# Kernel tuning notes

Measured on AMD Instinct MI355X. Metric: run time of the kernel, lower is better.

The kernel has to match this reference:

```python
import jax, jax.numpy as jnp
import numpy as np

N_NODES = 20000
N_EDGES = 320000
IN_F = 168
HID = 256


def gcn_conv(x, W, b, src, dst, ew, n_nodes):
    """PyG GCNConv: symmetric normalization with self-loops (fill 1.0).
    out = D^-1/2 (A + I) D^-1/2 X W^T + b, aggregated at dst (source_to_target).
    """
    xw = x @ W.T  # [N, F_out]
    # degree at target nodes, including self-loop weight 1.0
    deg = jax.ops.segment_sum(ew, dst, num_segments=n_nodes) + 1.0
    dinv = jnp.where(deg > 0, jax.lax.rsqrt(deg), 0.0)
    norm = dinv[src] * ew * dinv[dst]  # [E]
    agg = jax.ops.segment_sum(norm[:, None] * xw[src], dst, num_segments=n_nodes)
    # self-loop contribution: norm_ii = dinv[i]^2
    out = agg + (dinv * dinv)[:, None] * xw
    return out + b


def setup_inputs() -> dict:
    key = jax.random.key(0)
    k = jax.random.split(key, 8)
    x = jax.random.normal(k[0], (N_NODES, IN_F), dtype=jnp.float32)
    edge_index = jax.random.randint(k[1], (2, N_EDGES), 0, N_NODES, dtype=jnp.int64)
    edge_weight = jax.random.uniform(k[2], (N_EDGES,), dtype=jnp.float32)
    # GCN layer weights (PyG Linear: y = x W^T), plus per-layer bias
    s1 = 1.0 / np.sqrt(IN_F)
    s2 = 1.0 / np.sqrt(HID)
    W1 = jax.random.uniform(k[3], (HID, IN_F), minval=-s1, maxval=s1, dtype=jnp.float32)
    b1 = jnp.zeros((HID,), dtype=jnp.float32)
    W2 = jax.random.uniform(k[4], (HID, HID), minval=-s2, maxval=s2, dtype=jnp.float32)
    b2 = jnp.zeros((HID,), dtype=jnp.float32)
    return {"x": x, "edge_index": edge_index, "edge_weight": edge_weight,
            "W1": W1, "b1": b1, "W2": W2, "b2": b2}


def reference(x, edge_index, edge_weight, W1, b1, W2, b2):
    src, dst = edge_index[0], edge_index[1]
    h = gcn_conv(x, W1, b1, src, dst, edge_weight, N_NODES)
    h = jax.nn.relu(h)
    h = gcn_conv(h, W2, b2, src, dst, edge_weight, N_NODES)
    h = jax.nn.relu(h)
    return h
```

## Files before the change

### kernel.cpp

```cpp
#include <hip/hip_runtime.h>

#define N_NODES 20000
#define N_EDGES 320000
#define IN_F    168
#define HID     256
#define K1P     192
#define XS      192
#define NF4     42
#define X4      48
#define CAP     96
#define E2      (N_EDGES / 2)

typedef __attribute__((ext_vector_type(8))) short bf16x8;
typedef __attribute__((ext_vector_type(4))) float f32x4;
typedef __attribute__((ext_vector_type(2))) float f32x2;

__device__ __forceinline__ short f2bf(float f) {
    union { float f; unsigned u; } v; v.f = f;
    unsigned r = v.u + 0x7FFFu + ((v.u >> 16) & 1u);
    return (short)(r >> 16);
}
__device__ __forceinline__ f32x2 bfp(unsigned u) {
    f32x2 r;
    r.x = __uint_as_float(u << 16);
    r.y = __uint_as_float(u & 0xFFFF0000u);
    return r;
}

__global__ void prep_all(const float* __restrict__ x, short* __restrict__ xb,
                         const float* __restrict__ W1, const float* __restrict__ W2,
                         short* __restrict__ w1b, short* __restrict__ w2b,
                         const int* __restrict__ ei, const float* __restrict__ ew,
                         float* __restrict__ deg, int* __restrict__ counts) {
    const int xTot  = N_NODES * X4;
    const int w1Tot = 256 * X4;
    const int w2Tot = 256 * 64;
    int i = blockIdx.x * 256 + threadIdx.x;
    if (i < xTot) {
        int n  = i / X4;
        int k4 = i - n * X4;
        short4 o;
        if (k4 < NF4) {
            float4 v = *(const float4*)(x + (size_t)n * IN_F + k4 * 4);
            o = make_short4(f2bf(v.x), f2bf(v.y), f2bf(v.z), f2bf(v.w));
        } else {
            o = make_short4(0, 0, 0, 0);
        }
        *(short4*)(xb + (size_t)n * XS + k4 * 4) = o;
        return;
    }
    i -= xTot;
    if (i < w1Tot) {
        int r  = i / X4;
        int k4 = i - r * X4;
        short4 o;
        if (k4 < NF4) {
            float4 v = *(const float4*)(W1 + (size_t)r * IN_F + k4 * 4);
            o = make_short4(f2bf(v.x), f2bf(v.y), f2bf(v.z), f2bf(v.w));
        } else {
            o = make_short4(0, 0, 0, 0);
        }
        *(short4*)(w1b + (size_t)r * K1P + k4 * 4) = o;
        return;
    }
    i -= w1Tot;
    if (i < w2Tot) {
        int r  = i >> 6;
        int c4 = i & 63;
        float4 v = *(const float4*)(W2 + (size_t)r * HID + c4 * 4);
        *(short4*)(w2b + (size_t)r * HID + c4 * 4) =
            make_short4(f2bf(v.x), f2bf(v.y), f2bf(v.z), f2bf(v.w));
        return;
    }
    i -= w2Tot;
    if (i < N_EDGES) {
        int d = ei[N_EDGES + i];
        atomicAdd(&deg[d], ew[i]);
        atomicAdd(&counts[d], 1);
    }
}

__global__ void scatter_edges(const int* __restrict__ ei, const float* __restrict__ ew,
                              const float* __restrict__ deg,
                              const int* __restrict__ counts,
                              int* __restrict__ cursor, int2* __restrict__ er) {
    int t = blockIdx.x * 256 + threadIdx.x;
    if (t < E2) {
        int2   s2 = *(const int2*)(ei + 2 * t);
        int2   d2 = *(const int2*)(ei + N_EDGES + 2 * t);
        float2 w2 = *(const float2*)(ew + 2 * t);
        float nm0 = rsqrtf(deg[s2.x] + 1.0f) * w2.x * rsqrtf(deg[d2.x] + 1.0f);
        int c0 = atomicAdd(&cursor[d2.x], 1);
        if (c0 < CAP) er[d2.x * CAP + c0] = make_int2(s2.x, __float_as_int(nm0));
        float nm1 = rsqrtf(deg[s2.y] + 1.0f) * w2.y * rsqrtf(deg[d2.y] + 1.0f);
        int c1 = atomicAdd(&cursor[d2.y], 1);
        if (c1 < CAP) er[d2.y * CAP + c1] = make_int2(s2.y, __float_as_int(nm1));
        return;
    }
    int n = t - E2;
    if (n < N_NODES) {
        int base = n * CAP;
        int p   = base + counts[n];
        int end = base + ((counts[n] + 7) & ~7);
        for (; p < end; ++p) er[p] = make_int2(0, 0);
    }
}


__global__ __launch_bounds__(256) void agg_x(const short* __restrict__ xb,
                                             const float* __restrict__ deg,
                                             const int* __restrict__ counts,
                                             const int2* __restrict__ er,
                                             short* __restrict__ ax) {
    int wave = threadIdx.x >> 6;
    int lane = threadIdx.x & 63;
    int n = blockIdx.x * 4 + wave;
    bool act = lane < NF4;
    int lo4 = act ? lane * 4 : 0;
    float di = rsqrtf(deg[n] + 1.0f);
    float sw = di * di;
    uint2 sv = *(const uint2*)(xb + (size_t)n * XS + lo4);
    f32x2 a01 = bfp(sv.x) * sw;
    f32x2 a23 = bfp(sv.y) * sw;

    int p0 = n * CAP;
    int p1 = p0 + ((counts[n] + 7) & ~7);
    for (int p = p0; p < p1; p += 8) {
        const int4* e4 = (const int4*)(er + p);
        int4 eA = e4[0], eB = e4[1], eC = e4[2], eD = e4[3];
        uint2 r0 = *(const uint2*)(xb + (size_t)eA.x * XS + lo4);
        uint2 r1 = *(const uint2*)(xb + (size_t)eA.z * XS + lo4);
        uint2 r2 = *(const uint2*)(xb + (size_t)eB.x * XS + lo4);
        uint2 r3 = *(const uint2*)(xb + (size_t)eB.z * XS + lo4);
        uint2 r4 = *(const uint2*)(xb + (size_t)eC.x * XS + lo4);
        uint2 r5 = *(const uint2*)(xb + (size_t)eC.z * XS + lo4);
        uint2 r6 = *(const uint2*)(xb + (size_t)eD.x * XS + lo4);
        uint2 r7 = *(const uint2*)(xb + (size_t)eD.z * XS + lo4);
        float w0 = __int_as_float(eA.y), w1 = __int_as_float(eA.w);
        float w2 = __int_as_float(eB.y), w3 = __int_as_float(eB.w);
        float w4 = __int_as_float(eC.y), w5 = __int_as_float(eC.w);
        float w6 = __int_as_float(eD.y), w7 = __int_as_float(eD.w);
        a01 += bfp(r0.x) * w0; a23 += bfp(r0.y) * w0;
        a01 += bfp(r1.x) * w1; a23 += bfp(r1.y) * w1;
        a01 += bfp(r2.x) * w2; a23 += bfp(r2.y) * w2;
        a01 += bfp(r3.x) * w3; a23 += bfp(r3.y) * w3;
        a01 += bfp(r4.x) * w4; a23 += bfp(r4.y) * w4;
        a01 += bfp(r5.x) * w5; a23 += bfp(r5.y) * w5;
        a01 += bfp(r6.x) * w6; a23 += bfp(r6.y) * w6;
        a01 += bfp(r7.x) * w7; a23 += bfp(r7.y) * w7;
    }

    size_t base = (size_t)n * K1P + lane * 4;
    if (act) {
        *(short4*)&ax[base] = make_short4(f2bf(a01.x), f2bf(a01.y),
                                          f2bf(a23.x), f2bf(a23.y));
    } else if (lane < 48) {
        *(short4*)&ax[base] = make_short4(0, 0, 0, 0);
    }
}

__global__ __launch_bounds__(256) void agg_h(const short* __restrict__ h1h,
                                             const float* __restrict__ deg,
                                             const int* __restrict__ counts,
                                             const int2* __restrict__ er,
                                             short* __restrict__ ah) {
    int wave = threadIdx.x >> 6;
    int lane = threadIdx.x & 63;
    int n = blockIdx.x * 4 + wave;
    int lo4 = lane * 4;
    float di = rsqrtf(deg[n] + 1.0f);
    float sw = di * di;
    uint2 sv = *(const uint2*)(h1h + (size_t)n * HID + lo4);
    f32x2 a01 = bfp(sv.x) * sw;
    f32x2 a23 = bfp(sv.y) * sw;

    int p0 = n * CAP;
    int p1 = p0 + ((counts[n] + 7) & ~7);
    for (int p = p0; p < p1; p += 8) {
        const int4* e4 = (const int4*)(er + p);
        int4 eA = e4[0], eB = e4[1], eC = e4[2], eD = e4[3];
        uint2 r0 = *(const uint2*)(h1h + (size_t)eA.x * HID + lo4);
        uint2 r1 = *(const uint2*)(h1h + (size_t)eA.z * HID + lo4);
        uint2 r2 = *(const uint2*)(h1h + (size_t)eB.x * HID + lo4);
        uint2 r3 = *(const uint2*)(h1h + (size_t)eB.z * HID + lo4);
        uint2 r4 = *(const uint2*)(h1h + (size_t)eC.x * HID + lo4);
        uint2 r5 = *(const uint2*)(h1h + (size_t)eC.z * HID + lo4);
        uint2 r6 = *(const uint2*)(h1h + (size_t)eD.x * HID + lo4);
        uint2 r7 = *(const uint2*)(h1h + (size_t)eD.z * HID + lo4);
        float w0 = __int_as_float(eA.y), w1 = __int_as_float(eA.w);
        float w2 = __int_as_float(eB.y), w3 = __int_as_float(eB.w);
        float w4 = __int_as_float(eC.y), w5 = __int_as_float(eC.w);
        float w6 = __int_as_float(eD.y), w7 = __int_as_float(eD.w);
        a01 += bfp(r0.x) * w0; a23 += bfp(r0.y) * w0;
        a01 += bfp(r1.x) * w1; a23 += bfp(r1.y) * w1;
        a01 += bfp(r2.x) * w2; a23 += bfp(r2.y) * w2;
        a01 += bfp(r3.x) * w3; a23 += bfp(r3.y) * w3;
        a01 += bfp(r4.x) * w4; a23 += bfp(r4.y) * w4;
        a01 += bfp(r5.x) * w5; a23 += bfp(r5.y) * w5;
        a01 += bfp(r6.x) * w6; a23 += bfp(r6.y) * w6;
        a01 += bfp(r7.x) * w7; a23 += bfp(r7.y) * w7;
    }

    *(short4*)&ah[(size_t)n * HID + lo4] = make_short4(f2bf(a01.x), f2bf(a01.y),
                                                       f2bf(a23.x), f2bf(a23.y));
}

#define LDS_STRIDE 72

__global__ __launch_bounds__(256) void gemm_bf(const short* __restrict__ Ah,
                                               const short* __restrict__ Wh,
                                               const float* __restrict__ bias,
                                               float* __restrict__ Cf,
                                               short* __restrict__ Cbf,
                                               int M, int Ks, int nsteps, int mode) {
    __shared__ short sAh[64 * LDS_STRIDE];
    __shared__ short sWh[64 * LDS_STRIDE];

    const int idx   = blockIdx.x;
    const int group = idx >> 5;
    const int xcd   = idx & 7;
    const int slot  = (idx >> 3) & 3;
    const int mt    = group * 8 + xcd;
    const int mtiles = (M + 63) >> 6;
    if (mt >= mtiles) return;
    const int bm = mt * 64;
    const int bn = slot * 64;

    const int tid  = threadIdx.x;
    const int lane = tid & 63;
    const int wv   = tid >> 6;
    const int l16  = lane & 15;
    const int quad = lane >> 4;
    const int wm   = (wv & 1) * 32;
    const int wn   = (wv >> 1) * 32;

    const int srow = tid >> 2;
    const int sseg = (tid & 3) * 16;
    int arow = bm + srow; if (arow >= M) arow = M - 1;
    const short* gAh = Ah + (size_t)arow * Ks;
    const short* gWh = Wh + (size_t)(bn + srow) * Ks;
    const int lds_off = srow * LDS_STRIDE + sseg;

    f32x4 acc00 = {0,0,0,0}, acc01 = {0,0,0,0}, acc10 = {0,0,0,0}, acc11 = {0,0,0,0};

    int4 pah0 = *(const int4*)(gAh + sseg), pah1 = *(const int4*)(gAh + sseg + 8);
    int4 pwh0 = *(const int4*)(gWh + sseg), pwh1 = *(const int4*)(gWh + sseg + 8);

    for (int ks = 0; ks < nsteps; ++ks) {
        *(int4*)&sAh[lds_off] = pah0; *(int4*)&sAh[lds_off + 8] = pah1;
        *(int4*)&sWh[lds_off] = pwh0; *(int4*)&sWh[lds_off + 8] = pwh1;
        __syncthreads();
        if (ks + 1 < nsteps) {
            int o = (ks + 1) * 64 + sseg;
            pah0 = *(const int4*)(gAh + o); pah1 = *(const int4*)(gAh + o + 8);
            pwh0 = *(const int4*)(gWh + o); pwh1 = *(const int4*)(gWh + o + 8);
        }
        #pragma unroll
        for (int o = 0; o < 2; ++o) {
            const int a0 = (wm + l16) * LDS_STRIDE + o * 32 + quad * 8;
            const int a1 = a0 + 16 * LDS_STRIDE;
            const int w0 = (wn + l16) * LDS_STRIDE + o * 32 + quad * 8;
            const int w1 = w0 + 16 * LDS_STRIDE;
            bf16x8 ah0 = *(const bf16x8*)&sAh[a0];
            bf16x8 ah1 = *(const bf16x8*)&sAh[a1];
            bf16x8 wh0 = *(const bf16x8*)&sWh[w0];
            bf16x8 wh1 = *(const bf16x8*)&sWh[w1];
            acc00 = __builtin_amdgcn_mfma_f32_16x16x32_bf16(ah0, wh0, acc00, 0, 0, 0);
            acc01 = __builtin_amdgcn_mfma_f32_16x16x32_bf16(ah0, wh1, acc01, 0, 0, 0);
            acc10 = __builtin_amdgcn_mfma_f32_16x16x32_bf16(ah1, wh0, acc10, 0, 0, 0);
            acc11 = __builtin_amdgcn_mfma_f32_16x16x32_bf16(ah1, wh1, acc11, 0, 0, 0);
        }
        __syncthreads();
    }

    const int colb = bn + wn + l16;
    const int rowb = bm + wm + quad * 4;
    const float b0 = bias[colb];
    const float b1 = bias[colb + 16];
    #pragma unroll
    for (int r = 0; r < 4; ++r) {
        int row = rowb + r;
        if (row < M) {
            float v0 = acc00[r] + b0; v0 = v0 > 0.f ? v0 : 0.f;
            float v1 = acc01[r] + b1; v1 = v1 > 0.f ? v1 : 0.f;
            if (mode == 0) {
                Cbf[(size_t)row * HID + colb]      = f2bf(v0);
                Cbf[(size_t)row * HID + colb + 16] = f2bf(v1);
            } else {
                Cf[(size_t)row * HID + colb]      = v0;
                Cf[(size_t)row * HID + colb + 16] = v1;
            }
        }
        int row2 = row + 16;
        if (row2 < M) {
            float v0 = acc10[r] + b0; v0 = v0 > 0.f ? v0 : 0.f;
            float v1 = acc11[r] + b1; v1 = v1 > 0.f ? v1 : 0.f;
            if (mode == 0) {
                Cbf[(size_t)row2 * HID + colb]      = f2bf(v0);
                Cbf[(size_t)row2 * HID + colb + 16] = f2bf(v1);
            } else {
                Cf[(size_t)row2 * HID + colb]      = v0;
                Cf[(size_t)row2 * HID + colb + 16] = v1;
            }
        }
    }
}


extern "C" void kernel_launch(void* const* d_in, const int* in_sizes, int n_in,
                              void* d_out, int out_size, void* d_ws, size_t ws_size,
                              hipStream_t stream) {
    const float* x  = (const float*)d_in[0];
    const int*   ei = (const int*)d_in[1];
    const float* ew = (const float*)d_in[2];
    const float* W1 = (const float*)d_in[3];
    const float* b1 = (const float*)d_in[4];
    const float* W2 = (const float*)d_in[5];
    const float* b2 = (const float*)d_in[6];
    float* out = (float*)d_out;

    char* ws = (char*)d_ws;
    float* deg      = (float*)(ws);
    int*   counts   = (int*)(ws + 80000);
    int*   cursor   = (int*)(ws + 160000);
    int2*  er       = (int2*)(ws + 240000);
    short* ax       = (short*)(ws + 15600000);
    short* ah       = (short*)(ws + 15600000);
    short* h1h      = (short*)(ws + 25840000);
    short* w1b      = (short*)(ws + 36080000);
    short* w2b      = (short*)(ws + 36178304);
    short* xb       = (short*)(ws + 36309376);

    hipMemsetAsync(d_ws, 0, 240000, stream);

    const int prep_tot = N_NODES * X4 + 256 * X4 + 256 * 64 + N_EDGES;
    prep_all<<<(prep_tot + 255) / 256, 256, 0, stream>>>(
        x, xb, W1, W2, w1b, w2b, ei, ew, deg, counts);
    const int sc_blocks = (E2 + N_NODES + 255) / 256;
    scatter_edges<<<sc_blocks, 256, 0, stream>>>(ei, ew, deg, counts, cursor, er);

    const int mtiles = (N_NODES + 63) / 64;
    const int gemm_grid = ((mtiles + 7) / 8) * 32;

    agg_x<<<N_NODES / 4, 256, 0, stream>>>(xb, deg, counts, er, ax);
    gemm_bf<<<gemm_grid, 256, 0, stream>>>(ax, w1b, b1, nullptr, h1h,
                                           N_NODES, K1P, 3, 0);
    agg_h<<<N_NODES / 4, 256, 0, stream>>>(h1h, deg, counts, er, ah);
    gemm_bf<<<gemm_grid, 256, 0, stream>>>(ah, w2b, b2, out, nullptr,
                                           N_NODES, HID, 4, 1);
}
```

Baseline: 191.7 us.

## Fuse neighbor aggregation with dense GEMM per 16-row tile for both layers

Replaces the separate aggregate kernels and tiled GEMM kernels with two fused kernels. Each block aggregates 16 nodes into LDS as bf16 and then multiplies them by the weight matrix with MFMA, reading weight fragments directly from global memory. This removes the round trip of the aggregated matrices through global memory and cuts two kernel launches. In exchange, weights are re-read by every block without LDS staging, and each wave now processes its 4 rows sequentially, which reduces gather parallelism.

New measurement: 207.5 us. 1.08x slower.

```diff
diff --git a/kernel.cpp b/kernel.cpp
--- a/kernel.cpp
+++ b/kernel.cpp
@@ -10,6 +10,8 @@
 #define X4      48
 #define CAP     96
 #define E2      (N_EDGES / 2)
+#define ASTR1   200
+#define ASTR2   264
 
 typedef __attribute__((ext_vector_type(8))) short bf16x8;
 typedef __attribute__((ext_vector_type(4))) float f32x4;
@@ -106,203 +108,186 @@
     }
 }
 
-
-__global__ __launch_bounds__(256) void agg_x(const short* __restrict__ xb,
-                                             const float* __restrict__ deg,
-                                             const int* __restrict__ counts,
-                                             const int2* __restrict__ er,
-                                             short* __restrict__ ax) {
-    int wave = threadIdx.x >> 6;
-    int lane = threadIdx.x & 63;
-    int n = blockIdx.x * 4 + wave;
-    bool act = lane < NF4;
-    int lo4 = act ? lane * 4 : 0;
-    float di = rsqrtf(deg[n] + 1.0f);
-    float sw = di * di;
-    uint2 sv = *(const uint2*)(xb + (size_t)n * XS + lo4);
-    f32x2 a01 = bfp(sv.x) * sw;
-    f32x2 a23 = bfp(sv.y) * sw;
-
-    int p0 = n * CAP;
-    int p1 = p0 + ((counts[n] + 7) & ~7);
-    for (int p = p0; p < p1; p += 8) {
-        const int4* e4 = (const int4*)(er + p);
-        int4 eA = e4[0], eB = e4[1], eC = e4[2], eD = e4[3];
-        uint2 r0 = *(const uint2*)(xb + (size_t)eA.x * XS + lo4);
-        uint2 r1 = *(const uint2*)(xb + (size_t)eA.z * XS + lo4);
-        uint2 r2 = *(const uint2*)(xb + (size_t)eB.x * XS + lo4);
-        uint2 r3 = *(const uint2*)(xb + (size_t)eB.z * XS + lo4);
-        uint2 r4 = *(const uint2*)(xb + (size_t)eC.x * XS + lo4);
-        uint2 r5 = *(const uint2*)(xb + (size_t)eC.z * XS + lo4);
-        uint2 r6 = *(const uint2*)(xb + (size_t)eD.x * XS + lo4);
-        uint2 r7 = *(const uint2*)(xb + (size_t)eD.z * XS + lo4);
-        float w0 = __int_as_float(eA.y), w1 = __int_as_float(eA.w);
-        float w2 = __int_as_float(eB.y), w3 = __int_as_float(eB.w);
-        float w4 = __int_as_float(eC.y), w5 = __int_as_float(eC.w);
-        float w6 = __int_as_float(eD.y), w7 = __int_as_float(eD.w);
-        a01 += bfp(r0.x) * w0; a23 += bfp(r0.y) * w0;
-        a01 += bfp(r1.x) * w1; a23 += bfp(r1.y) * w1;
-        a01 += bfp(r2.x) * w2; a23 += bfp(r2.y) * w2;
-        a01 += bfp(r3.x) * w3; a23 += bfp(r3.y) * w3;
-        a01 += bfp(r4.x) * w4; a23 += bfp(r4.y) * w4;
-        a01 += bfp(r5.x) * w5; a23 += bfp(r5.y) * w5;
-        a01 += bfp(r6.x) * w6; a23 += bfp(r6.y) * w6;
-        a01 += bfp(r7.x) * w7; a23 += bfp(r7.y) * w7;
-    }
-
-    size_t base = (size_t)n * K1P + lane * 4;
-    if (act) {
-        *(short4*)&ax[base] = make_short4(f2bf(a01.x), f2bf(a01.y),
-                                          f2bf(a23.x), f2bf(a23.y));
-    } else if (lane < 48) {
-        *(short4*)&ax[base] = make_short4(0, 0, 0, 0);
-    }
-}
-
-__global__ __launch_bounds__(256) void agg_h(const short* __restrict__ h1h,
-                                             const float* __restrict__ deg,
-                                             const int* __restrict__ counts,
-                                             const int2* __restrict__ er,
-                                             short* __restrict__ ah) {
-    int wave = threadIdx.x >> 6;
-    int lane = threadIdx.x & 63;
-    int n = blockIdx.x * 4 + wave;
-    int lo4 = lane * 4;
-    float di = rsqrtf(deg[n] + 1.0f);
-    float sw = di * di;
-    uint2 sv = *(const uint2*)(h1h + (size_t)n * HID + lo4);
-    f32x2 a01 = bfp(sv.x) * sw;
-    f32x2 a23 = bfp(sv.y) * sw;
-
-    int p0 = n * CAP;
-    int p1 = p0 + ((counts[n] + 7) & ~7);
-    for (int p = p0; p < p1; p += 8) {
-        const int4* e4 = (const int4*)(er + p);
-        int4 eA = e4[0], eB = e4[1], eC = e4[2], eD = e4[3];
-        uint2 r0 = *(const uint2*)(h1h + (size_t)eA.x * HID + lo4);
-        uint2 r1 = *(const uint2*)(h1h + (size_t)eA.z * HID + lo4);
-        uint2 r2 = *(const uint2*)(h1h + (size_t)eB.x * HID + lo4);
-        uint2 r3 = *(const uint2*)(h1h + (size_t)eB.z * HID + lo4);
-        uint2 r4 = *(const uint2*)(h1h + (size_t)eC.x * HID + lo4);
-        uint2 r5 = *(const uint2*)(h1h + (size_t)eC.z * HID + lo4);
-        uint2 r6 = *(const uint2*)(h1h + (size_t)eD.x * HID + lo4);
-        uint2 r7 = *(const uint2*)(h1h + (size_t)eD.z * HID + lo4);
-        float w0 = __int_as_float(eA.y), w1 = __int_as_float(eA.w);
-        float w2 = __int_as_float(eB.y), w3 = __int_as_float(eB.w);
-        float w4 = __int_as_float(eC.y), w5 = __int_as_float(eC.w);
-        float w6 = __int_as_float(eD.y), w7 = __int_as_float(eD.w);
-        a01 += bfp(r0.x) * w0; a23 += bfp(r0.y) * w0;
-        a01 += bfp(r1.x) * w1; a23 += bfp(r1.y) * w1;
-        a01 += bfp(r2.x) * w2; a23 += bfp(r2.y) * w2;
-        a01 += bfp(r3.x) * w3; a23 += bfp(r3.y) * w3;
-        a01 += bfp(r4.x) * w4; a23 += bfp(r4.y) * w4;
-        a01 += bfp(r5.x) * w5; a23 += bfp(r5.y) * w5;
-        a01 += bfp(r6.x) * w6; a23 += bfp(r6.y) * w6;
-        a01 += bfp(r7.x) * w7; a23 += bfp(r7.y) * w7;
-    }
-
-    *(short4*)&ah[(size_t)n * HID + lo4] = make_short4(f2bf(a01.x), f2bf(a01.y),
-                                                       f2bf(a23.x), f2bf(a23.y));
-}
-
-#define LDS_STRIDE 72
-
-__global__ __launch_bounds__(256) void gemm_bf(const short* __restrict__ Ah,
-                                               const short* __restrict__ Wh,
-                                               const float* __restrict__ bias,
-                                               float* __restrict__ Cf,
-                                               short* __restrict__ Cbf,
-                                               int M, int Ks, int nsteps, int mode) {
-    __shared__ short sAh[64 * LDS_STRIDE];
-    __shared__ short sWh[64 * LDS_STRIDE];
-
-    const int idx   = blockIdx.x;
-    const int group = idx >> 5;
-    const int xcd   = idx & 7;
-    const int slot  = (idx >> 3) & 3;
-    const int mt    = group * 8 + xcd;
-    const int mtiles = (M + 63) >> 6;
-    if (mt >= mtiles) return;
-    const int bm = mt * 64;
-    const int bn = slot * 64;
-
+__global__ __launch_bounds__(256) void fused1(
+    const short* __restrict__ xb, const float* __restrict__ deg,
+    const int* __restrict__ counts, const int2* __restrict__ er,
+    const short* __restrict__ w1b, const float* __restrict__ b1,
+    short* __restrict__ h1h)
+{
+    __shared__ short sA[16 * ASTR1];
     const int tid  = threadIdx.x;
+    const int wave = tid >> 6;
     const int lane = tid & 63;
-    const int wv   = tid >> 6;
+
+    {
+        bool act = lane < NF4;
+        int lo4 = act ? lane * 4 : 0;
+        for (int i = 0; i < 4; ++i) {
+            int r = wave * 4 + i;
+            int n = blockIdx.x * 16 + r;
+            float di = rsqrtf(deg[n] + 1.0f);
+            float sw = di * di;
+            uint2 sv = *(const uint2*)(xb + (size_t)n * XS + lo4);
+            f32x2 a01 = bfp(sv.x) * sw;
+            f32x2 a23 = bfp(sv.y) * sw;
+            int p0 = n * CAP;
+            int p1 = p0 + ((counts[n] + 7) & ~7);
+            for (int p = p0; p < p1; p += 8) {
+                const int4* e4 = (const int4*)(er + p);
+                int4 eA = e4[0], eB = e4[1], eC = e4[2], eD = e4[3];
+                uint2 r0 = *(const uint2*)(xb + (size_t)eA.x * XS + lo4);
+                uint2 r1 = *(const uint2*)(xb + (size_t)eA.z * XS + lo4);
+                uint2 r2 = *(const uint2*)(xb + (size_t)eB.x * XS + lo4);
+                uint2 r3 = *(const uint2*)(xb + (size_t)eB.z * XS + lo4);
+                uint2 r4 = *(const uint2*)(xb + (size_t)eC.x * XS + lo4);
+                uint2 r5 = *(const uint2*)(xb + (size_t)eC.z * XS + lo4);
+                uint2 r6 = *(const uint2*)(xb + (size_t)eD.x * XS + lo4);
+                uint2 r7 = *(const uint2*)(xb + (size_t)eD.z * XS + lo4);
+                float w0 = __int_as_float(eA.y), w1 = __int_as_float(eA.w);
+                float w2 = __int_as_float(eB.y), w3 = __int_as_float(eB.w);
+                float w4 = __int_as_float(eC.y), w5 = __int_as_float(eC.w);
+                float w6 = __int_as_float(eD.y), w7 = __int_as_float(eD.w);
+                a01 += bfp(r0.x) * w0; a23 += bfp(r0.y) * w0;
+                a01 += bfp(r1.x) * w1; a23 += bfp(r1.y) * w1;
+                a01 += bfp(r2.x) * w2; a23 += bfp(r2.y) * w2;
+                a01 += bfp(r3.x) * w3; a23 += bfp(r3.y) * w3;
+                a01 += bfp(r4.x) * w4; a23 += bfp(r4.y) * w4;
+                a01 += bfp(r5.x) * w5; a23 += bfp(r5.y) * w5;
+                a01 += bfp(r6.x) * w6; a23 += bfp(r6.y) * w6;
+                a01 += bfp(r7.x) * w7; a23 += bfp(r7.y) * w7;
+            }
+            if (act) {
+                *(short4*)&sA[r * ASTR1 + lane * 4] =
+                    make_short4(f2bf(a01.x), f2bf(a01.y), f2bf(a23.x), f2bf(a23.y));
+            } else if (lane < 48) {
+                *(short4*)&sA[r * ASTR1 + lane * 4] = make_short4(0, 0, 0, 0);
+            }
+        }
+    }
+    __syncthreads();
+
     const int l16  = lane & 15;
     const int quad = lane >> 4;
-    const int wm   = (wv & 1) * 32;
-    const int wn   = (wv >> 1) * 32;
-
-    const int srow = tid >> 2;
-    const int sseg = (tid & 3) * 16;
-    int arow = bm + srow; if (arow >= M) arow = M - 1;
-    const short* gAh = Ah + (size_t)arow * Ks;
-    const short* gWh = Wh + (size_t)(bn + srow) * Ks;
-    const int lds_off = srow * LDS_STRIDE + sseg;
-
-    f32x4 acc00 = {0,0,0,0}, acc01 = {0,0,0,0}, acc10 = {0,0,0,0}, acc11 = {0,0,0,0};
-
-    int4 pah0 = *(const int4*)(gAh + sseg), pah1 = *(const int4*)(gAh + sseg + 8);
-    int4 pwh0 = *(const int4*)(gWh + sseg), pwh1 = *(const int4*)(gWh + sseg + 8);
-
-    for (int ks = 0; ks < nsteps; ++ks) {
-        *(int4*)&sAh[lds_off] = pah0; *(int4*)&sAh[lds_off + 8] = pah1;
-        *(int4*)&sWh[lds_off] = pwh0; *(int4*)&sWh[lds_off + 8] = pwh1;
-        __syncthreads();
-        if (ks + 1 < nsteps) {
-            int o = (ks + 1) * 64 + sseg;
-            pah0 = *(const int4*)(gAh + o); pah1 = *(const int4*)(gAh + o + 8);
-            pwh0 = *(const int4*)(gWh + o); pwh1 = *(const int4*)(gWh + o + 8);
-        }
-        #pragma unroll
-        for (int o = 0; o < 2; ++o) {
-            const int a0 = (wm + l16) * LDS_STRIDE + o * 32 + quad * 8;
-            const int a1 = a0 + 16 * LDS_STRIDE;
-            const int w0 = (wn + l16) * LDS_STRIDE + o * 32 + quad * 8;
-            const int w1 = w0 + 16 * LDS_STRIDE;
-            bf16x8 ah0 = *(const bf16x8*)&sAh[a0];
-            bf16x8 ah1 = *(const bf16x8*)&sAh[a1];
-            bf16x8 wh0 = *(const bf16x8*)&sWh[w0];
-            bf16x8 wh1 = *(const bf16x8*)&sWh[w1];
-            acc00 = __builtin_amdgcn_mfma_f32_16x16x32_bf16(ah0, wh0, acc00, 0, 0, 0);
-            acc01 = __builtin_amdgcn_mfma_f32_16x16x32_bf16(ah0, wh1, acc01, 0, 0, 0);
-            acc10 = __builtin_amdgcn_mfma_f32_16x16x32_bf16(ah1, wh0, acc10, 0, 0, 0);
-            acc11 = __builtin_amdgcn_mfma_f32_16x16x32_bf16(ah1, wh1, acc11, 0, 0, 0);
-        }
-        __syncthreads();
-    }
-
-    const int colb = bn + wn + l16;
-    const int rowb = bm + wm + quad * 4;
-    const float b0 = bias[colb];
-    const float b1 = bias[colb + 16];
+    const int wc   = wave * 64;
+    f32x4 acc0 = {0,0,0,0}, acc1 = {0,0,0,0}, acc2 = {0,0,0,0}, acc3 = {0,0,0,0};
+    const short* wp0 = w1b + (size_t)(wc + l16) * K1P + quad * 8;
+    for (int ks = 0; ks < 6; ++ks) {
+        int ko = ks * 32;
+        bf16x8 af  = *(const bf16x8*)&sA[l16 * ASTR1 + ko + quad * 8];
+        bf16x8 wf0 = *(const bf16x8*)(wp0 + ko);
+        bf16x8 wf1 = *(const bf16x8*)(wp0 + 16 * K1P + ko);
+        bf16x8 wf2 = *(const bf16x8*)(wp0 + 32 * K1P + ko);
+        bf16x8 wf3 = *(const bf16x8*)(wp0 + 48 * K1P + ko);
+        acc0 = __builtin_amdgcn_mfma_f32_16x16x32_bf16(af, wf0, acc0, 0, 0, 0);
+        acc1 = __builtin_amdgcn_mfma_f32_16x16x32_bf16(af, wf1, acc1, 0, 0, 0);
+        acc2 = __builtin_amdgcn_mfma_f32_16x16x32_bf16(af, wf2, acc2, 0, 0, 0);
+        acc3 = __builtin_amdgcn_mfma_f32_16x16x32_bf16(af, wf3, acc3, 0, 0, 0);
+    }
+    const int row0 = blockIdx.x * 16 + quad * 4;
+    const float bb0 = b1[wc + l16];
+    const float bb1 = b1[wc + 16 + l16];
+    const float bb2 = b1[wc + 32 + l16];
+    const float bb3 = b1[wc + 48 + l16];
     #pragma unroll
     for (int r = 0; r < 4; ++r) {
-        int row = rowb + r;
-        if (row < M) {
-            float v0 = acc00[r] + b0; v0 = v0 > 0.f ? v0 : 0.f;
-            float v1 = acc01[r] + b1; v1 = v1 > 0.f ? v1 : 0.f;
-            if (mode == 0) {
-                Cbf[(size_t)row * HID + colb]      = f2bf(v0);
-                Cbf[(size_t)row * HID + colb + 16] = f2bf(v1);
-            } else {
-                Cf[(size_t)row * HID + colb]      = v0;
-                Cf[(size_t)row * HID + colb + 16] = v1;
+        size_t rb = (size_t)(row0 + r) * HID + wc + l16;
+        float v0 = acc0[r] + bb0; v0 = v0 > 0.f ? v0 : 0.f;
+        float v1 = acc1[r] + bb1; v1 = v1 > 0.f ? v1 : 0.f;
+        float v2 = acc2[r] + bb2; v2 = v2 > 0.f ? v2 : 0.f;
+        float v3 = acc3[r] + bb3; v3 = v3 > 0.f ? v3 : 0.f;
+        h1h[rb]      = f2bf(v0);
+        h1h[rb + 16] = f2bf(v1);
+        h1h[rb + 32] = f2bf(v2);
+        h1h[rb + 48] = f2bf(v3);
+    }
+}
+
+__global__ __launch_bounds__(256) void fused2(
+    const short* __restrict__ h1h, const float* __restrict__ deg,
+    const int* __restrict__ counts, const int2* __restrict__ er,
+    const short* __restrict__ w2b, const float* __restrict__ b2,
+    float* __restrict__ out)
+{
+    __shared__ short sA[16 * ASTR2];
+    const int tid  = threadIdx.x;
+    const int wave = tid >> 6;
+    const int lane = tid & 63;
+
+    {
+        int lo4 = lane * 4;
+        for (int i = 0; i < 4; ++i) {
+            int r = wave * 4 + i;
+            int n = blockIdx.x * 16 + r;
+            float di = rsqrtf(deg[n] + 1.0f);
+            float sw = di * di;
+            uint2 sv = *(const uint2*)(h1h + (size_t)n * HID + lo4);
+            f32x2 a01 = bfp(sv.x) * sw;
+            f32x2 a23 = bfp(sv.y) * sw;
+            int p0 = n * CAP;
+            int p1 = p0 + ((counts[n] + 7) & ~7);
+            for (int p = p0; p < p1; p += 8) {
+                const int4* e4 = (const int4*)(er + p);
+                int4 eA = e4[0], eB = e4[1], eC = e4[2], eD = e4[3];
+                uint2 r0 = *(const uint2*)(h1h + (size_t)eA.x * HID + lo4);
+                uint2 r1 = *(const uint2*)(h1h + (size_t)eA.z * HID + lo4);
+                uint2 r2 = *(const uint2*)(h1h + (size_t)eB.x * HID + lo4);
+                uint2 r3 = *(const uint2*)(h1h + (size_t)eB.z * HID + lo4);
+                uint2 r4 = *(const uint2*)(h1h + (size_t)eC.x * HID + lo4);
+                uint2 r5 = *(const uint2*)(h1h + (size_t)eC.z * HID + lo4);
+                uint2 r6 = *(const uint2*)(h1h + (size_t)eD.x * HID + lo4);
+                uint2 r7 = *(const uint2*)(h1h + (size_t)eD.z * HID + lo4);
+                float w0 = __int_as_float(eA.y), w1 = __int_as_float(eA.w);
+                float w2 = __int_as_float(eB.y), w3 = __int_as_float(eB.w);
+                float w4 = __int_as_float(eC.y), w5 = __int_as_float(eC.w);
+                float w6 = __int_as_float(eD.y), w7 = __int_as_float(eD.w);
+                a01 += bfp(r0.x) * w0; a23 += bfp(r0.y) * w0;
+                a01 += bfp(r1.x) * w1; a23 += bfp(r1.y) * w1;
+                a01 += bfp(r2.x) * w2; a23 += bfp(r2.y) * w2;
+                a01 += bfp(r3.x) * w3; a23 += bfp(r3.y) * w3;
+                a01 += bfp(r4.x) * w4; a23 += bfp(r4.y) * w4;
+                a01 += bfp(r5.x) * w5; a23 += bfp(r5.y) * w5;
+                a01 += bfp(r6.x) * w6; a23 += bfp(r6.y) * w6;
+                a01 += bfp(r7.x) * w7; a23 += bfp(r7.y) * w7;
             }
+            *(short4*)&sA[r * ASTR2 + lo4] =
+                make_short4(f2bf(a01.x), f2bf(a01.y), f2bf(a23.x), f2bf(a23.y));
         }
-        int row2 = row + 16;
-        if (row2 < M) {
-            float v0 = acc10[r] + b0; v0 = v0 > 0.f ? v0 : 0.f;
-            float v1 = acc11[r] + b1; v1 = v1 > 0.f ? v1 : 0.f;
-            if (mode == 0) {
-                Cbf[(size_t)row2 * HID + colb]      = f2bf(v0);
-                Cbf[(size_t)row2 * HID + colb + 16] = f2bf(v1);
-            } else {
-                Cf[(size_t)row2 * HID + colb]      = v0;
-                Cf[(size_t)row2 * HID + colb + 16] = v1;
-            }
-        }
+    }
+    __syncthreads();
+
+    const int l16 = lane & 15;
+    const int q   = lane >> 4;
+    const int wc  = wave * 64;
+    f32x4 acc0 = {0,0,0,0}, acc1 = {0,0,0,0}, acc2 = {0,0,0,0}, acc3 = {0,0,0,0};
+    const short* wp0 = w2b + (size_t)(wc + l16) * HID + q * 8;
+    for (int ks = 0; ks < 8; ++ks) {
+        int ko = ks * 32;
+        bf16x8 af  = *(const bf16x8*)&sA[l16 * ASTR2 + ko + q * 8];
+        bf16x8 wf0 = *(const bf16x8*)(wp0 + ko);
+        bf16x8 wf1 = *(const bf16x8*)(wp0 + 16 * HID + ko);
+        bf16x8 wf2 = *(const bf16x8*)(wp0 + 32 * HID + ko);
+        bf16x8 wf3 = *(const bf16x8*)(wp0 + 48 * HID + ko);
+        acc0 = __builtin_amdgcn_mfma_f32_16x16x32_bf16(af, wf0, acc0, 0, 0, 0);
+        acc1 = __builtin_amdgcn_mfma_f32_16x16x32_bf16(af, wf1, acc1, 0, 0, 0);
+        acc2 = __builtin_amdgcn_mfma_f32_16x16x32_bf16(af, wf2, acc2, 0, 0, 0);
+        acc3 = __builtin_amdgcn_mfma_f32_16x16x32_bf16(af, wf3, acc3, 0, 0, 0);
+    }
+    const int row0 = blockIdx.x * 16 + q * 4;
+    const float bb0 = b2[wc + l16];
+    const float bb1 = b2[wc + 16 + l16];
+    const float bb2 = b2[wc + 32 + l16];
+    const float bb3 = b2[wc + 48 + l16];
+    #pragma unroll
+    for (int r = 0; r < 4; ++r) {
+        size_t rb = (size_t)(row0 + r) * HID + wc + l16;
+        float v0 = acc0[r] + bb0; v0 = v0 > 0.f ? v0 : 0.f;
+        float v1 = acc1[r] + bb1; v1 = v1 > 0.f ? v1 : 0.f;
+        float v2 = acc2[r] + bb2; v2 = v2 > 0.f ? v2 : 0.f;
+        float v3 = acc3[r] + bb3; v3 = v3 > 0.f ? v3 : 0.f;
+        out[rb]      = v0;
+        out[rb + 16] = v1;
+        out[rb + 32] = v2;
+        out[rb + 48] = v3;
     }
 }
 
@@ -324,12 +309,10 @@
     int*   counts   = (int*)(ws + 80000);
     int*   cursor   = (int*)(ws + 160000);
     int2*  er       = (int2*)(ws + 240000);
-    short* ax       = (short*)(ws + 15600000);
-    short* ah       = (short*)(ws + 15600000);
-    short* h1h      = (short*)(ws + 25840000);
-    short* w1b      = (short*)(ws + 36080000);
-    short* w2b      = (short*)(ws + 36178304);
-    short* xb       = (short*)(ws + 36309376);
+    short* h1h      = (short*)(ws + 15600000);
+    short* w1b      = (short*)(ws + 25840000);
+    short* w2b      = (short*)(ws + 25938304);
+    short* xb       = (short*)(ws + 26069376);
 
     hipMemsetAsync(d_ws, 0, 240000, stream);
 
@@ -339,13 +322,7 @@
     const int sc_blocks = (E2 + N_NODES + 255) / 256;
     scatter_edges<<<sc_blocks, 256, 0, stream>>>(ei, ew, deg, counts, cursor, er);
 
-    const int mtiles = (N_NODES + 63) / 64;
-    const int gemm_grid = ((mtiles + 7) / 8) * 32;
-
-    agg_x<<<N_NODES / 4, 256, 0, stream>>>(xb, deg, counts, er, ax);
-    gemm_bf<<<gemm_grid, 256, 0, stream>>>(ax, w1b, b1, nullptr, h1h,
-                                           N_NODES, K1P, 3, 0);
-    agg_h<<<N_NODES / 4, 256, 0, stream>>>(h1h, deg, counts, er, ah);
-    gemm_bf<<<gemm_grid, 256, 0, stream>>>(ah, w2b, b2, out, nullptr,
-                                           N_NODES, HID, 4, 1);
-}
+    const int ftiles = N_NODES / 16;
+    fused1<<<ftiles, 256, 0, stream>>>(xb, deg, counts, er, w1b, b1, h1h);
+    fused2<<<ftiles, 256, 0, stream>>>(h1h, deg, counts, er, w2b, b2, out);
+}
```
